# Performance work log

Hardware: AMD Instinct MI355X
Metric: run time of the kernel (lower is better)

The kernel has to match this reference:

```python
import jax, jax.numpy as jnp
import numpy as np

B, S, E, H = 4, 1024, 1024, 16
HD = E // H  # head_dim = 64


def setup_inputs() -> dict:
    key = jax.random.key(0)
    ks = jax.random.split(key, 7)
    return {
        "query": jax.random.normal(ks[0], (B, S, E), dtype=jnp.float32),
        "key": jax.random.normal(ks[1], (B, S, E), dtype=jnp.float32),
        "value": jax.random.normal(ks[2], (B, S, E), dtype=jnp.float32),
        # per-head Linear weights stacked: [H, head_dim, emb_dim] (torch Linear is y = x @ W^T)
        "Wq": jax.random.normal(ks[3], (H, HD, E), dtype=jnp.float32) * (E ** -0.5),
        "Wk": jax.random.normal(ks[4], (H, HD, E), dtype=jnp.float32) * (E ** -0.5),
        "Wv": jax.random.normal(ks[5], (H, HD, E), dtype=jnp.float32) * (E ** -0.5),
        "Wo": jax.random.normal(ks[6], (E, E), dtype=jnp.float32) * (E ** -0.5),
    }


def reference(query, key, value, Wq, Wk, Wv, Wo):
    # Project per head (all heads vectorized): [B,S,E] x [H,HD,E] -> [B,H,S,HD]
    Q = jnp.einsum('bse,hde->bhsd', query, Wq)
    K = jnp.einsum('bse,hde->bhsd', key, Wk)
    V = jnp.einsum('bse,hde->bhsd', value, Wv)
    scale = 1.0 / np.sqrt(HD)  # source divides by sqrt(emb_dim / n_head)
    scores = jnp.einsum('bhsd,bhtd->bhst', Q, K) * scale  # [B,H,S,S]
    p = jax.nn.softmax(scores, axis=-1)
    ctx = jnp.einsum('bhst,bhtd->bhsd', p, V)  # [B,H,S,HD]
    # concat heads along feature dim -> [B,S,E]
    concat = ctx.transpose(0, 2, 1, 3).reshape(query.shape[0], query.shape[1], -1)
    return concat @ Wo.T
```

## Files before the change

### kernel.cpp

```cpp
#include <hip/hip_runtime.h>

typedef __bf16 bf16_t;
typedef __bf16 bf16x4 __attribute__((ext_vector_type(4)));
typedef __bf16 bf16x8 __attribute__((ext_vector_type(8)));
typedef float f32x4 __attribute__((ext_vector_type(4)));
typedef short short4v __attribute__((ext_vector_type(4)));

#define E_DIM 1024
#define S_LEN 1024
#define NHEAD 16
#define HD_DIM 64
#define BATCH 4
#define TOKENS 4096

__device__ __forceinline__ void async_copy16(const bf16_t* g, bf16_t* l) {
    __builtin_amdgcn_global_load_lds((const __attribute__((address_space(1))) void*)g,
                                     (__attribute__((address_space(3))) void*)l,
                                     16, 0, 0);
}

__device__ __forceinline__ f32x4 pv_mfma(bf16x4 a, bf16x4 b, f32x4 c) {
#if __has_builtin(__builtin_amdgcn_mfma_f32_16x16x16_bf16)
    return __builtin_amdgcn_mfma_f32_16x16x16_bf16(a, b, c, 0, 0, 0);
#elif __has_builtin(__builtin_amdgcn_mfma_f32_16x16x16bf16_1k)
    short4v as, bs;
    __builtin_memcpy(&as, &a, 8);
    __builtin_memcpy(&bs, &b, 8);
    return __builtin_amdgcn_mfma_f32_16x16x16bf16_1k(as, bs, c, 0, 0, 0);
#else
    f32x4 d;
    asm volatile("v_mfma_f32_16x16x16_bf16 %0, %1, %2, %3\n\ts_nop 7\n\ts_nop 7"
                 : "=v"(d)
                 : "v"(a), "v"(b), "v"(c));
    return d;
#endif
}

__global__ __launch_bounds__(256) void cast_all(const float* __restrict__ q,
                                                const float* __restrict__ k,
                                                const float* __restrict__ v,
                                                const float* __restrict__ wq,
                                                const float* __restrict__ wk,
                                                const float* __restrict__ wv,
                                                const float* __restrict__ wo,
                                                bf16_t* __restrict__ dst) {
    const size_t NX = (size_t)TOKENS * E_DIM;
    const size_t NW = (size_t)E_DIM * E_DIM;
    size_t i = ((size_t)blockIdx.x * 256 + threadIdx.x) * 8;
    const float* src;
    size_t off;
    if (i < 3 * NX) {
        int a = (int)(i >> 22);
        src = a == 0 ? q : (a == 1 ? k : v);
        off = i & (NX - 1);
    } else {
        size_t j = i - 3 * NX;
        int a = (int)(j >> 20);
        src = a == 0 ? wq : (a == 1 ? wk : (a == 2 ? wv : wo));
        off = j & (NW - 1);
    }
    float4 x = *(const float4*)(src + off);
    float4 y = *(const float4*)(src + off + 4);
    bf16x8 o;
    o[0] = (bf16_t)x.x; o[1] = (bf16_t)x.y; o[2] = (bf16_t)x.z; o[3] = (bf16_t)x.w;
    o[4] = (bf16_t)y.x; o[5] = (bf16_t)y.y; o[6] = (bf16_t)y.z; o[7] = (bf16_t)y.w;
    *(bf16x8*)(dst + i) = o;
}

__global__ __launch_bounds__(256, 4) void proj_gemm(const bf16_t* __restrict__ Xq,
                                                    const bf16_t* __restrict__ Xk,
                                                    const bf16_t* __restrict__ Xv,
                                                    const bf16_t* __restrict__ Wq,
                                                    const bf16_t* __restrict__ Wk,
                                                    const bf16_t* __restrict__ Wv,
                                                    bf16_t* __restrict__ Qp,
                                                    bf16_t* __restrict__ Kp,
                                                    bf16_t* __restrict__ Vp) {
    __shared__ bf16_t sA[128 * 32];
    __shared__ bf16_t sB[128 * 32];
    const int z = blockIdx.z;
    const bf16_t* A = z == 0 ? Xq : (z == 1 ? Xk : Xv);
    const bf16_t* B = z == 0 ? Wq : (z == 1 ? Wk : Wv);
    bf16_t* C = z == 0 ? Qp : (z == 1 ? Kp : Vp);
    const int N = 1024, K = 1024;
    const int lid = blockIdx.x + 8 * blockIdx.y;
    const int m0 = (((lid & 7) << 2) + ((lid >> 3) & 3)) * 128;
    const int n0 = (lid >> 5) * 128;

    const int tid = threadIdx.x;
    const int wave = tid >> 6, lane = tid & 63;
    const int quad = lane >> 4, l16 = lane & 15;
    const int wm = (wave >> 1) * 64, wn = (wave & 1) * 64;
    const int srow = lane >> 2, scol = (lane & 3) * 8;

    f32x4 acc[4][4];
    const f32x4 vzero = {0.f, 0.f, 0.f, 0.f};
#pragma unroll
    for (int mt = 0; mt < 4; mt++)
#pragma unroll
        for (int nt = 0; nt < 4; nt++) acc[mt][nt] = vzero;

    for (int k0 = 0; k0 < K; k0 += 32) {
        __syncthreads();
#pragma unroll
        for (int cc = 0; cc < 4; cc++) {
            int c = wave * 4 + cc;
            const bf16_t* g;
            bf16_t* l;
            if (c < 8) {
                g = A + (size_t)(m0 + c * 16 + srow) * K + k0 + scol;
                l = &sA[c * 16 * 32];
            } else {
                g = B + (size_t)(n0 + (c - 8) * 16 + srow) * K + k0 + scol;
                l = &sB[(c - 8) * 16 * 32];
            }
            async_copy16(g, l);
        }
        asm volatile("s_waitcnt vmcnt(0)" ::: "memory");
        __syncthreads();

        bf16x8 af[4], bfr[4];
#pragma unroll
        for (int mt = 0; mt < 4; mt++)
            af[mt] = *(const bf16x8*)&sA[(wm + mt * 16 + l16) * 32 + quad * 8];
#pragma unroll
        for (int nt = 0; nt < 4; nt++)
            bfr[nt] = *(const bf16x8*)&sB[(wn + nt * 16 + l16) * 32 + quad * 8];
#pragma unroll
        for (int mt = 0; mt < 4; mt++)
#pragma unroll
            for (int nt = 0; nt < 4; nt++)
                acc[mt][nt] = __builtin_amdgcn_mfma_f32_16x16x32_bf16(af[mt], bfr[nt],
                                                                      acc[mt][nt], 0, 0, 0);
    }

#pragma unroll
    for (int mt = 0; mt < 4; mt++)
#pragma unroll
        for (int nt = 0; nt < 4; nt++)
#pragma unroll
            for (int r = 0; r < 4; r++) {
                int row = m0 + wm + mt * 16 + quad * 4 + r;
                int col = n0 + wn + nt * 16 + l16;
                C[(size_t)row * N + col] = (bf16_t)acc[mt][nt][r];
            }
}

__global__ __launch_bounds__(256, 4) void out_gemm(const bf16_t* __restrict__ A,
                                                   const bf16_t* __restrict__ B,
                                                   float* __restrict__ C) {
    __shared__ bf16_t sA[128 * 32];
    __shared__ bf16_t sB[128 * 32];
    const int N = 1024, K = 1024;
    const int lid = blockIdx.x + 8 * blockIdx.y;
    const int m0 = (((lid & 7) << 2) + ((lid >> 3) & 3)) * 128;
    const int n0 = (lid >> 5) * 128;

    const int tid = threadIdx.x;
    const int wave = tid >> 6, lane = tid & 63;
    const int quad = lane >> 4, l16 = lane & 15;
    const int wm = (wave >> 1) * 64, wn = (wave & 1) * 64;
    const int srow = lane >> 2, scol = (lane & 3) * 8;

    f32x4 acc[4][4];
    const f32x4 vzero = {0.f, 0.f, 0.f, 0.f};
#pragma unroll
    for (int mt = 0; mt < 4; mt++)
#pragma unroll
        for (int nt = 0; nt < 4; nt++) acc[mt][nt] = vzero;

    for (int k0 = 0; k0 < K; k0 += 32) {
        __syncthreads();
#pragma unroll
        for (int cc = 0; cc < 4; cc++) {
            int c = wave * 4 + cc;
            const bf16_t* g;
            bf16_t* l;
            if (c < 8) {
                g = A + (size_t)(m0 + c * 16 + srow) * K + k0 + scol;
                l = &sA[c * 16 * 32];
            } else {
                g = B + (size_t)(n0 + (c - 8) * 16 + srow) * K + k0 + scol;
                l = &sB[(c - 8) * 16 * 32];
            }
            async_copy16(g, l);
        }
        asm volatile("s_waitcnt vmcnt(0)" ::: "memory");
        __syncthreads();

        bf16x8 af[4], bfr[4];
#pragma unroll
        for (int mt = 0; mt < 4; mt++)
            af[mt] = *(const bf16x8*)&sA[(wm + mt * 16 + l16) * 32 + quad * 8];
#pragma unroll
        for (int nt = 0; nt < 4; nt++)
            bfr[nt] = *(const bf16x8*)&sB[(wn + nt * 16 + l16) * 32 + quad * 8];
#pragma unroll
        for (int mt = 0; mt < 4; mt++)
#pragma unroll
            for (int nt = 0; nt < 4; nt++)
                acc[mt][nt] = __builtin_amdgcn_mfma_f32_16x16x32_bf16(af[mt], bfr[nt],
                                                                      acc[mt][nt], 0, 0, 0);
    }

#pragma unroll
    for (int mt = 0; mt < 4; mt++)
#pragma unroll
        for (int nt = 0; nt < 4; nt++)
#pragma unroll
            for (int r = 0; r < 4; r++) {
                int row = m0 + wm + mt * 16 + quad * 4 + r;
                int col = n0 + wn + nt * 16 + l16;
                C[(size_t)row * N + col] = acc[mt][nt][r];
            }
}

#define KP 72

__global__ __launch_bounds__(256, 2) void flash_attn(const bf16_t* __restrict__ Q,
                                                     const bf16_t* __restrict__ K,
                                                     const bf16_t* __restrict__ V,
                                                     bf16_t* __restrict__ O) {
    __shared__ bf16_t smem[2 * 64 * KP];
    bf16_t* sK = smem;
    bf16_t* sVt = smem + 64 * KP;

    const int tid = threadIdx.x;
    const int wave = tid >> 6, lane = tid & 63;
    const int quad = lane >> 4, l16 = lane & 15;
    const int qt = blockIdx.y >> 1;
    const int h = blockIdx.x * 2 + (blockIdx.y & 1);
    const int b = blockIdx.z;
    const size_t base = (size_t)b * S_LEN * E_DIM + h * HD_DIM;
    const float c_exp = 0.125f * 1.44269504089f;

    bf16x8 qf[2][2];
#pragma unroll
    for (int mt = 0; mt < 2; mt++) {
        const bf16_t* qp =
            Q + base + (size_t)(qt * 128 + wave * 32 + mt * 16 + l16) * E_DIM + quad * 8;
        qf[mt][0] = *(const bf16x8*)qp;
        qf[mt][1] = *(const bf16x8*)(qp + 32);
    }

    float lsum[2] = {0.f, 0.f};
    f32x4 acc[2][4];
    const f32x4 vzero = {0.f, 0.f, 0.f, 0.f};
#pragma unroll
    for (int mt = 0; mt < 2; mt++)
#pragma unroll
        for (int dt = 0; dt < 4; dt++) acc[mt][dt] = vzero;

    const int stg = tid & 7;

    for (int j0 = 0; j0 < S_LEN; j0 += 64) {
        __syncthreads();
#pragma unroll
        for (int it = 0; it < 2; it++) {
            int r = (tid >> 3) + it * 32;
            int c = stg * 8;
            bf16x8 kv = *(const bf16x8*)(K + base + (size_t)(j0 + r) * E_DIM + c);
            *(bf16x8*)&sK[r * KP + c] = kv;
            bf16x8 vv = *(const bf16x8*)(V + base + (size_t)(j0 + r) * E_DIM + c);
            int jb = (((r >> 2) ^ stg) << 2) | (r & 3);
#pragma unroll
            for (int i = 0; i < 8; i++) sVt[(c + i) * KP + jb] = vv[i];
        }
        __syncthreads();

        bf16x8 kf[4][2];
#pragma unroll
        for (int jt = 0; jt < 4; jt++) {
            kf[jt][0] = *(const bf16x8*)&sK[(jt * 16 + l16) * KP + quad * 8];
            kf[jt][1] = *(const bf16x8*)&sK[(jt * 16 + l16) * KP + 32 + quad * 8];
        }

        bf16x4 pb[2][4];
#pragma unroll
        for (int mt = 0; mt < 2; mt++)
#pragma unroll
            for (int jt = 0; jt < 4; jt++) {
                f32x4 s = vzero;
                s = __builtin_amdgcn_mfma_f32_16x16x32_bf16(kf[jt][0], qf[mt][0], s, 0, 0, 0);
                s = __builtin_amdgcn_mfma_f32_16x16x32_bf16(kf[jt][1], qf[mt][1], s, 0, 0, 0);
#pragma unroll
                for (int r = 0; r < 4; r++) {
                    float p = __builtin_amdgcn_exp2f(s[r] * c_exp);
                    lsum[mt] += p;
                    pb[mt][jt][r] = (bf16_t)p;
                }
            }

#pragma unroll
        for (int jt = 0; jt < 4; jt++)
#pragma unroll
            for (int dt = 0; dt < 4; dt++) {
                int cidx = (jt * 4 + quad) ^ (dt * 2 + (l16 >> 3));
                bf16x4 vf = *(const bf16x4*)&sVt[(dt * 16 + l16) * KP + cidx * 4];
#pragma unroll
                for (int mt = 0; mt < 2; mt++)
                    acc[mt][dt] = pv_mfma(vf, pb[mt][jt], acc[mt][dt]);
            }
    }

    float inv[2];
#pragma unroll
    for (int mt = 0; mt < 2; mt++) {
        lsum[mt] += __shfl_xor(lsum[mt], 16);
        lsum[mt] += __shfl_xor(lsum[mt], 32);
        inv[mt] = __builtin_amdgcn_rcpf(lsum[mt]);
    }

    __syncthreads();
    bf16_t* ep = smem + wave * 32 * KP;
#pragma unroll
    for (int mt = 0; mt < 2; mt++)
#pragma unroll
        for (int dt = 0; dt < 4; dt++)
#pragma unroll
            for (int r = 0; r < 4; r++)
                ep[(mt * 16 + l16) * KP + dt * 16 + quad * 4 + r] =
                    (bf16_t)(acc[mt][dt][r] * inv[mt]);
#pragma unroll
    for (int mt = 0; mt < 2; mt++)
#pragma unroll
        for (int c = 0; c < 2; c++) {
            int row = lane >> 2;
            int col = (lane & 3) * 8 + c * 32;
            bf16x8 oval = *(const bf16x8*)&ep[(mt * 16 + row) * KP + col];
            *(bf16x8*)&O[base + (size_t)(qt * 128 + wave * 32 + mt * 16 + row) * E_DIM + col] =
                oval;
        }
}

extern "C" void kernel_launch(void* const* d_in, const int* in_sizes, int n_in,
                              void* d_out, int out_size, void* d_ws, size_t ws_size,
                              hipStream_t stream) {
    const float* q  = (const float*)d_in[0];
    const float* k  = (const float*)d_in[1];
    const float* v  = (const float*)d_in[2];
    const float* wq = (const float*)d_in[3];
    const float* wk = (const float*)d_in[4];
    const float* wv = (const float*)d_in[5];
    const float* wo = (const float*)d_in[6];
    float* out = (float*)d_out;

    const int NX = TOKENS * E_DIM;
    const int NW = E_DIM * E_DIM;

    bf16_t* ws  = (bf16_t*)d_ws;
    bf16_t* Xq  = ws;
    bf16_t* Xk  = ws + (size_t)NX;
    bf16_t* Xv  = ws + (size_t)2 * NX;
    bf16_t* Wqb = ws + (size_t)3 * NX;
    bf16_t* Wkb = Wqb + NW;
    bf16_t* Wvb = Wkb + NW;
    bf16_t* Wob = Wvb + NW;
    bf16_t* Qp  = Wob + NW;
    bf16_t* Kp  = Qp + (size_t)NX;
    bf16_t* Vp  = Kp + (size_t)NX;
    bf16_t* ctx = Xq;

    cast_all<<<8192, 256, 0, stream>>>(q, k, v, wq, wk, wv, wo, Xq);

    proj_gemm<<<dim3(8, 32, 3), 256, 0, stream>>>(Xq, Xk, Xv, Wqb, Wkb, Wvb, Qp, Kp, Vp);

    flash_attn<<<dim3(8, 16, 4), 256, 0, stream>>>(Qp, Kp, Vp, ctx);

    out_gemm<<<dim3(8, 32), 256, 0, stream>>>(ctx, Wob, out);
}
```

Before: 193.6 us.

## Double-buffer LDS tiles in projection and output GEMMs to overlap loads with MFMA

Both GEMM kernels now use two LDS buffers per operand and prefetch the next K-slice with async global-to-LDS copies while computing MFMAs on the current one. This halves the barriers per iteration and hides global load latency behind compute. LDS use doubles to 32 KB per block, which may limit occupancy against the launch bound of 4 blocks per CU.

```diff
diff --git a/kernel.cpp b/kernel.cpp
--- a/kernel.cpp
+++ b/kernel.cpp
@@ -34,6 +34,20 @@
                  : "v"(a), "v"(b), "v"(c));
     return d;
 #endif
+}
+
+__device__ __forceinline__ void stage_tiles(const bf16_t* gA, const bf16_t* gB,
+                                            bf16_t* sAbuf, bf16_t* sBbuf,
+                                            int wave, int k0) {
+    const int K = 1024;
+#pragma unroll
+    for (int cc = 0; cc < 4; cc++) {
+        int c = wave * 4 + cc;
+        if (c < 8)
+            async_copy16(gA + (size_t)c * 16 * K + k0, sAbuf + c * 16 * 32);
+        else
+            async_copy16(gB + (size_t)(c - 8) * 16 * K + k0, sBbuf + (c - 8) * 16 * 32);
+    }
 }
 
 __global__ __launch_bounds__(256) void cast_all(const float* __restrict__ q,
@@ -76,8 +90,8 @@
                                                     bf16_t* __restrict__ Qp,
                                                     bf16_t* __restrict__ Kp,
                                                     bf16_t* __restrict__ Vp) {
-    __shared__ bf16_t sA[128 * 32];
-    __shared__ bf16_t sB[128 * 32];
+    __shared__ bf16_t sA[2][128 * 32];
+    __shared__ bf16_t sB[2][128 * 32];
     const int z = blockIdx.z;
     const bf16_t* A = z == 0 ? Xq : (z == 1 ? Xk : Xv);
     const bf16_t* B = z == 0 ? Wq : (z == 1 ? Wk : Wv);
@@ -93,6 +107,9 @@
     const int wm = (wave >> 1) * 64, wn = (wave & 1) * 64;
     const int srow = lane >> 2, scol = (lane & 3) * 8;
 
+    const bf16_t* gA = A + (size_t)(m0 + srow) * K + scol;
+    const bf16_t* gB = B + (size_t)(n0 + srow) * K + scol;
+
     f32x4 acc[4][4];
     const f32x4 vzero = {0.f, 0.f, 0.f, 0.f};
 #pragma unroll
@@ -100,32 +117,41 @@
 #pragma unroll
         for (int nt = 0; nt < 4; nt++) acc[mt][nt] = vzero;
 
-    for (int k0 = 0; k0 < K; k0 += 32) {
-        __syncthreads();
-#pragma unroll
-        for (int cc = 0; cc < 4; cc++) {
-            int c = wave * 4 + cc;
-            const bf16_t* g;
-            bf16_t* l;
-            if (c < 8) {
-                g = A + (size_t)(m0 + c * 16 + srow) * K + k0 + scol;
-                l = &sA[c * 16 * 32];
-            } else {
-                g = B + (size_t)(n0 + (c - 8) * 16 + srow) * K + k0 + scol;
-                l = &sB[(c - 8) * 16 * 32];
-            }
-            async_copy16(g, l);
-        }
+    stage_tiles(gA, gB, sA[0], sB[0], wave, 0);
+    asm volatile("s_waitcnt vmcnt(0)" ::: "memory");
+    __syncthreads();
+
+    int cur = 0;
+    for (int k0 = 32; k0 < K; k0 += 32) {
+        stage_tiles(gA, gB, sA[cur ^ 1], sB[cur ^ 1], wave, k0);
+
+        bf16x8 af[4], bfr[4];
+#pragma unroll
+        for (int mt = 0; mt < 4; mt++)
+            af[mt] = *(const bf16x8*)&sA[cur][(wm + mt * 16 + l16) * 32 + quad * 8];
+#pragma unroll
+        for (int nt = 0; nt < 4; nt++)
+            bfr[nt] = *(const bf16x8*)&sB[cur][(wn + nt * 16 + l16) * 32 + quad * 8];
+#pragma unroll
+        for (int mt = 0; mt < 4; mt++)
+#pragma unroll
+            for (int nt = 0; nt < 4; nt++)
+                acc[mt][nt] = __builtin_amdgcn_mfma_f32_16x16x32_bf16(af[mt], bfr[nt],
+                                                                      acc[mt][nt], 0, 0, 0);
+
         asm volatile("s_waitcnt vmcnt(0)" ::: "memory");
         __syncthreads();
-
+        cur ^= 1;
+    }
+
+    {
         bf16x8 af[4], bfr[4];
 #pragma unroll
         for (int mt = 0; mt < 4; mt++)
-            af[mt] = *(const bf16x8*)&sA[(wm + mt * 16 + l16) * 32 + quad * 8];
-#pragma unroll
-        for (int nt = 0; nt < 4; nt++)
-            bfr[nt] = *(const bf16x8*)&sB[(wn + nt * 16 + l16) * 32 + quad * 8];
+            af[mt] = *(const bf16x8*)&sA[cur][(wm + mt * 16 + l16) * 32 + quad * 8];
+#pragma unroll
+        for (int nt = 0; nt < 4; nt++)
+            bfr[nt] = *(const bf16x8*)&sB[cur][(wn + nt * 16 + l16) * 32 + quad * 8];
 #pragma unroll
         for (int mt = 0; mt < 4; mt++)
 #pragma unroll
@@ -149,8 +175,8 @@
 __global__ __launch_bounds__(256, 4) void out_gemm(const bf16_t* __restrict__ A,
                                                    const bf16_t* __restrict__ B,
                                                    float* __restrict__ C) {
-    __shared__ bf16_t sA[128 * 32];
-    __shared__ bf16_t sB[128 * 32];
+    __shared__ bf16_t sA[2][128 * 32];
+    __shared__ bf16_t sB[2][128 * 32];
     const int N = 1024, K = 1024;
     const int lid = blockIdx.x + 8 * blockIdx.y;
     const int m0 = (((lid & 7) << 2) + ((lid >> 3) & 3)) * 128;
@@ -162,6 +188,9 @@
     const int wm = (wave >> 1) * 64, wn = (wave & 1) * 64;
     const int srow = lane >> 2, scol = (lane & 3) * 8;
 
+    const bf16_t* gA = A + (size_t)(m0 + srow) * K + scol;
+    const bf16_t* gB = B + (size_t)(n0 + srow) * K + scol;
+
     f32x4 acc[4][4];
     const f32x4 vzero = {0.f, 0.f, 0.f, 0.f};
 #pragma unroll
@@ -169,32 +198,41 @@
 #pragma unroll
         for (int nt = 0; nt < 4; nt++) acc[mt][nt] = vzero;
 
-    for (int k0 = 0; k0 < K; k0 += 32) {
-        __syncthreads();
-#pragma unroll
-        for (int cc = 0; cc < 4; cc++) {
-            int c = wave * 4 + cc;
-            const bf16_t* g;
-            bf16_t* l;
-            if (c < 8) {
-                g = A + (size_t)(m0 + c * 16 + srow) * K + k0 + scol;
-                l = &sA[c * 16 * 32];
-            } else {
-                g = B + (size_t)(n0 + (c - 8) * 16 + srow) * K + k0 + scol;
-                l = &sB[(c - 8) * 16 * 32];
-            }
-            async_copy16(g, l);
-        }
+    stage_tiles(gA, gB, sA[0], sB[0], wave, 0);
+    asm volatile("s_waitcnt vmcnt(0)" ::: "memory");
+    __syncthreads();
+
+    int cur = 0;
+    for (int k0 = 32; k0 < K; k0 += 32) {
+        stage_tiles(gA, gB, sA[cur ^ 1], sB[cur ^ 1], wave, k0);
+
+        bf16x8 af[4], bfr[4];
+#pragma unroll
+        for (int mt = 0; mt < 4; mt++)
+            af[mt] = *(const bf16x8*)&sA[cur][(wm + mt * 16 + l16) * 32 + quad * 8];
+#pragma unroll
+        for (int nt = 0; nt < 4; nt++)
+            bfr[nt] = *(const bf16x8*)&sB[cur][(wn + nt * 16 + l16) * 32 + quad * 8];
+#pragma unroll
+        for (int mt = 0; mt < 4; mt++)
+#pragma unroll
+            for (int nt = 0; nt < 4; nt++)
+                acc[mt][nt] = __builtin_amdgcn_mfma_f32_16x16x32_bf16(af[mt], bfr[nt],
+                                                                      acc[mt][nt], 0, 0, 0);
+
         asm volatile("s_waitcnt vmcnt(0)" ::: "memory");
         __syncthreads();
-
+        cur ^= 1;
+    }
+
+    {
         bf16x8 af[4], bfr[4];
 #pragma unroll
         for (int mt = 0; mt < 4; mt++)
-            af[mt] = *(const bf16x8*)&sA[(wm + mt * 16 + l16) * 32 + quad * 8];
-#pragma unroll
-        for (int nt = 0; nt < 4; nt++)
-            bfr[nt] = *(const bf16x8*)&sB[(wn + nt * 16 + l16) * 32 + quad * 8];
+            af[mt] = *(const bf16x8*)&sA[cur][(wm + mt * 16 + l16) * 32 + quad * 8];
+#pragma unroll
+        for (int nt = 0; nt < 4; nt++)
+            bfr[nt] = *(const bf16x8*)&sB[cur][(wn + nt * 16 + l16) * 32 + quad * 8];
 #pragma unroll
         for (int mt = 0; mt < 4; mt++)
 #pragma unroll
```

Result: no change. 190.8 us (-1.5%).
